# Optimization experiments

Measured on AMD Instinct MI355X. Metric: run time of the kernel, lower is better.

## Reference

```python
import jax, jax.numpy as jnp
import numpy as np

# Module config (matches init_kwargs)
IN_CH, K, N_LAYERS, STRIDE = 4, 4, 2, 2
N_QUBITS = 6           # ceil(log2(4*4*4)) = 6
DIM = 2 ** N_QUBITS    # 64 amplitudes
B, H = 128, 128


def setup_inputs() -> dict:
    key = jax.random.key(0)
    k1, k2 = jax.random.split(key)
    x = jax.random.normal(k1, (B, IN_CH, H, H), dtype=jnp.float32)
    weights = jax.random.normal(k2, (N_LAYERS, N_QUBITS, 3), dtype=jnp.float32)
    return {"x": x, "weights": weights}


def _rot(phi, theta, omega):
    # PennyLane Rot(phi, theta, omega) = RZ(omega) RY(theta) RZ(phi)
    c = jnp.cos(theta / 2).astype(jnp.complex64)
    s = jnp.sin(theta / 2).astype(jnp.complex64)
    ep = jnp.exp(-0.5j * (phi + omega).astype(jnp.complex64))
    em = jnp.exp(-0.5j * (phi - omega).astype(jnp.complex64))
    row0 = jnp.stack([ep * c, -jnp.conj(em) * s])
    row1 = jnp.stack([em * s, jnp.conj(ep) * c])
    return jnp.stack([row0, row1])  # (2,2) complex64


def _apply_1q(state, U, w):
    # state: (N, 2,...,2); wire w -> axis 1+w (wire 0 most significant)
    s = jnp.moveaxis(state, 1 + w, -1)
    s = s @ U.T
    return jnp.moveaxis(s, -1, 1 + w)


def _apply_cnot(state, c, t):
    s = jnp.moveaxis(state, (1 + c, 1 + t), (1, 2))
    s = jnp.stack([s[:, 0], s[:, 1, ::-1]], axis=1)
    return jnp.moveaxis(s, (1, 2), (1 + c, 1 + t))


def _circuit(feat, weights):
    # feat: (N, DIM) amplitude-embedded & normalized features
    state = feat.astype(jnp.complex64).reshape((-1,) + (2,) * N_QUBITS)
    ranges = [(l % (N_QUBITS - 1)) + 1 for l in range(N_LAYERS)]
    for _rep in range(N_LAYERS):  # circuit applies the full template n_layers times
        for l in range(N_LAYERS):
            for w in range(N_QUBITS):
                U = _rot(weights[l, w, 0], weights[l, w, 1], weights[l, w, 2])
                state = _apply_1q(state, U, w)
            r = ranges[l]
            for w in range(N_QUBITS):
                state = _apply_cnot(state, w, (w + r) % N_QUBITS)
    probs = state.real ** 2 + state.imag ** 2
    z = []
    for w in range(N_QUBITS):
        p = jnp.moveaxis(probs, 1 + w, 1).reshape(probs.shape[0], 2, -1)
        z.append(p[:, 0].sum(-1) - p[:, 1].sum(-1))  # <Z_w>
    return jnp.stack(z, axis=1)  # (N, n_qubits)


def reference(x, weights):
    Bx, C, Hx, Wx = x.shape
    oh = (Hx - K) // STRIDE + 1
    idx = (jnp.arange(oh) * STRIDE)[:, None] + jnp.arange(K)  # (oh, K)
    p = x[:, :, idx, :]       # (B, C, oh, K, W)
    p = p[..., idx]           # (B, C, oh, K, oh, K)
    p = jnp.transpose(p, (0, 2, 4, 1, 3, 5)).reshape(Bx * oh * oh, C * K * K)
    feat = jnp.pad(p, ((0, 0), (0, DIM - C * K * K)))  # AmplitudeEmbedding pad_with=0
    feat = feat / jnp.linalg.norm(feat, axis=1, keepdims=True)  # normalize=True
    z = _circuit(feat, weights)                        # (B*oh*oh, n_qubits)
    out = z.reshape(Bx, oh, oh, N_QUBITS).transpose(0, 3, 1, 2)
    return out  # (B, n_qubits, oh, oh)
```

## Files before the change

### kernel.cpp

```cpp
#include <hip/hip_runtime.h>

#define NQ   6
#define DIM  64
#define OH   63
#define HH   128
#define CIN  4
#define NB   128
#define PSTR 80

typedef __attribute__((ext_vector_type(8))) short short8;
typedef __attribute__((ext_vector_type(4))) float f32x4;

__device__ __forceinline__ unsigned bf16_rne_u(float f) {
    unsigned u = __builtin_bit_cast(unsigned, f);
    return (u + 0x7fffu + ((u >> 16) & 1u)) >> 16;
}

#if __has_builtin(__builtin_amdgcn_cvt_pk_bf16_f32)
__device__ __forceinline__ unsigned pk_bf16(float a, float b) {
    typedef __attribute__((ext_vector_type(2))) __bf16 bf16x2_t;
    bf16x2_t v = __builtin_amdgcn_cvt_pk_bf16_f32(a, b);
    return __builtin_bit_cast(unsigned, v);
}
#else
__device__ __forceinline__ unsigned pk_bf16(float a, float b) {
    return bf16_rne_u(a) | (bf16_rne_u(b) << 16);
}
#endif

__global__ __launch_bounds__(64) void build_u(const float* __restrict__ wts,
                                              float2* __restrict__ Ut) {
    const int i   = threadIdx.x;
    const int col = blockIdx.x;
    float2 amp = make_float2(i == col ? 1.0f : 0.0f, 0.0f);
    const int ranges[2] = {1, 2};

    for (int rep = 0; rep < 2; ++rep) {
        for (int l = 0; l < 2; ++l) {
            for (int w = 0; w < NQ; ++w) {
                const float phi = wts[(l * NQ + w) * 3 + 0];
                const float th  = wts[(l * NQ + w) * 3 + 1];
                const float om  = wts[(l * NQ + w) * 3 + 2];
                const float hc = cosf(0.5f * th);
                const float hs = sinf(0.5f * th);
                const float ap = -0.5f * (phi + om);
                const float am = -0.5f * (phi - om);
                const float2 ep = make_float2(cosf(ap), sinf(ap));
                const float2 em = make_float2(cosf(am), sinf(am));
                const float2 U00 = make_float2( ep.x * hc,  ep.y * hc);
                const float2 U01 = make_float2(-em.x * hs,  em.y * hs);
                const float2 U10 = make_float2( em.x * hs,  em.y * hs);
                const float2 U11 = make_float2( ep.x * hc, -ep.y * hc);
                const int p = 5 - w;
                const int bbit = (i >> p) & 1;
                const float px = __shfl_xor(amp.x, 1 << p, 64);
                const float py = __shfl_xor(amp.y, 1 << p, 64);
                const float2 ua = bbit ? U11 : U00;
                const float2 ub = bbit ? U10 : U01;
                float2 na;
                na.x = ua.x * amp.x - ua.y * amp.y + ub.x * px - ub.y * py;
                na.y = ua.x * amp.y + ua.y * amp.x + ub.x * py + ub.y * px;
                amp = na;
            }
            const int r = ranges[l];
            for (int w = 0; w < NQ; ++w) {
                const int pc = 5 - w;
                const int pt = 5 - ((w + r) % NQ);
                const int src = i ^ (((i >> pc) & 1) << pt);
                const float nx = __shfl(amp.x, src, 64);
                const float ny = __shfl(amp.y, src, 64);
                amp = make_float2(nx, ny);
            }
        }
    }
    Ut[col * DIM + i] = amp;
}

__global__ __launch_bounds__(64) void wprep(const float2* __restrict__ Ut,
                                            short* __restrict__ wfrag) {
    const int f = blockIdx.x;
    const int l = threadIdx.x;
    const int mt = f >> 1;
    const int t  = f & 1;
    const int m  = mt * 16 + (l & 15);
    short8 v;
#pragma unroll
    for (int j = 0; j < 8; ++j) {
        const int k = t * 32 + (l >> 4) * 8 + j;
        const float2 u = Ut[k * DIM + (m & 63)];
        const float val = (m < 64) ? u.x : u.y;
        v[j] = (short)bf16_rne_u(val);
    }
    ((int4*)wfrag)[f * 64 + l] = __builtin_bit_cast(int4, v);
}

__global__ __launch_bounds__(256, 3) void qconv_mfma(const float* __restrict__ x,
                                                     const short* __restrict__ wfrag,
                                                     float* __restrict__ out) {
    __shared__ __align__(16) short sP[4][16 * PSTR];

    const int tid  = threadIdx.x;
    const int lane = tid & 63;
    const int wv   = tid >> 6;
    const int n    = lane & 15;
    const int qq   = lane >> 4;

    const int row = blockIdx.x * 4 + wv;
    const int b   = row / OH;
    const int oy  = row - b * OH;

    const int c0  = qq >> 1;
    const int kh0 = (qq & 1) * 2;
    const float* xb  = x + (size_t)b * CIN * HH * HH;
    const float* r00 = xb + ((c0    ) * HH + 2 * oy + kh0    ) * HH;
    const float* r01 = xb + ((c0    ) * HH + 2 * oy + kh0 + 1) * HH;
    const float* r10 = xb + ((c0 + 2) * HH + 2 * oy + kh0    ) * HH;
    const float* r11 = xb + ((c0 + 2) * HH + 2 * oy + kh0 + 1) * HH;

#define LOAD8(dst, ch_)                                                      \
    {                                                                        \
        const int oxl_ = min((ch_) * 16 + n, OH - 1);                        \
        const int fo_  = 2 * oxl_;                                           \
        dst[0] = *(const float2*)(r00 + fo_);                                \
        dst[1] = *(const float2*)(r00 + fo_ + 2);                            \
        dst[2] = *(const float2*)(r01 + fo_);                                \
        dst[3] = *(const float2*)(r01 + fo_ + 2);                            \
        dst[4] = *(const float2*)(r10 + fo_);                                \
        dst[5] = *(const float2*)(r10 + fo_ + 2);                            \
        dst[6] = *(const float2*)(r11 + fo_);                                \
        dst[7] = *(const float2*)(r11 + fo_ + 2);                            \
    }

    float2 cur[8];
    LOAD8(cur, 0)

    short8 wfr[8][2];
    {
        const int4* wp = (const int4*)wfrag;
#pragma unroll
        for (int mt = 0; mt < 8; ++mt)
#pragma unroll
            for (int t = 0; t < 2; ++t)
                wfr[mt][t] = __builtin_bit_cast(short8, wp[(mt * 2 + t) * 64 + lane]);
    }

    short8 sfr[2];
#pragma unroll
    for (int t = 0; t < 2; ++t) {
        short8 v;
#pragma unroll
        for (int j = 0; j < 8; ++j) {
            const int i = t * 32 + qq * 8 + j;
            unsigned short s;
            if (n < 6)       s = ((i >> (5 - n)) & 1) ? 0xBF80 : 0x3F80;
            else if (n == 6) s = 0x3F80;
            else             s = 0;
            v[j] = (short)s;
        }
        sfr[t] = v;
    }

    short* myP = sP[wv];

#pragma unroll
    for (int ch = 0; ch < 4; ++ch) {
        float2 nxt[8];
        if (ch < 3) LOAD8(nxt, ch + 1)

        uint4 u0, u1;
        u0.x = pk_bf16(cur[0].x, cur[0].y);  u0.y = pk_bf16(cur[1].x, cur[1].y);
        u0.z = pk_bf16(cur[2].x, cur[2].y);  u0.w = pk_bf16(cur[3].x, cur[3].y);
        u1.x = pk_bf16(cur[4].x, cur[4].y);  u1.y = pk_bf16(cur[5].x, cur[5].y);
        u1.z = pk_bf16(cur[6].x, cur[6].y);  u1.w = pk_bf16(cur[7].x, cur[7].y);
        const short8 bf0 = __builtin_bit_cast(short8, u0);
        const short8 bf1 = __builtin_bit_cast(short8, u1);

        f32x4 acc[8];
#pragma unroll
        for (int mt = 0; mt < 8; ++mt) acc[mt] = (f32x4){0.f, 0.f, 0.f, 0.f};
#pragma unroll
        for (int mt = 0; mt < 8; ++mt) {
            acc[mt] = __builtin_amdgcn_mfma_f32_16x16x32_bf16(wfr[mt][0], bf0, acc[mt], 0, 0, 0);
            acc[mt] = __builtin_amdgcn_mfma_f32_16x16x32_bf16(wfr[mt][1], bf1, acc[mt], 0, 0, 0);
        }

#pragma unroll
        for (int mt = 0; mt < 4; ++mt) {
            const float p0 = acc[mt][0] * acc[mt][0] + acc[mt + 4][0] * acc[mt + 4][0];
            const float p1 = acc[mt][1] * acc[mt][1] + acc[mt + 4][1] * acc[mt + 4][1];
            const float p2 = acc[mt][2] * acc[mt][2] + acc[mt + 4][2] * acc[mt + 4][2];
            const float p3 = acc[mt][3] * acc[mt][3] + acc[mt + 4][3] * acc[mt + 4][3];
            const unsigned w0 = pk_bf16(p0, p1);
            const unsigned w1 = pk_bf16(p2, p3);
            *((uint2*)(((unsigned*)myP) + n * (PSTR / 2) + mt * 8 + qq * 2)) =
                make_uint2(w0, w1);
        }

        const short8 p0f = *(const short8*)(myP + n * PSTR + qq * 8);
        const short8 p1f = *(const short8*)(myP + n * PSTR + 32 + qq * 8);
        f32x4 c2 = (f32x4){0.f, 0.f, 0.f, 0.f};
        c2 = __builtin_amdgcn_mfma_f32_16x16x32_bf16(sfr[0], p0f, c2, 0, 0, 0);
        c2 = __builtin_amdgcn_mfma_f32_16x16x32_bf16(sfr[1], p1f, c2, 0, 0, 0);

        const float norm = __shfl(c2[2], 16 + n, 64);
        const float inv  = 1.0f / norm;
        const int ox = ch * 16 + n;
        if (ox < OH) {
            float* ob = out + ((size_t)b * NQ * OH + oy) * OH + ox;
            if (qq == 0) {
#pragma unroll
                for (int r = 0; r < 4; ++r)
                    __builtin_nontemporal_store(c2[r] * inv, ob + (size_t)r * (OH * OH));
            } else if (qq == 1) {
                __builtin_nontemporal_store(c2[0] * inv, ob + (size_t)4 * (OH * OH));
                __builtin_nontemporal_store(c2[1] * inv, ob + (size_t)5 * (OH * OH));
            }
        }

        if (ch < 3) {
#pragma unroll
            for (int i = 0; i < 8; ++i) cur[i] = nxt[i];
        }
    }
#undef LOAD8
}

extern "C" void kernel_launch(void* const* d_in, const int* in_sizes, int n_in,
                              void* d_out, int out_size, void* d_ws, size_t ws_size,
                              hipStream_t stream) {
    const float* x   = (const float*)d_in[0];
    const float* wts = (const float*)d_in[1];
    float* out = (float*)d_out;

    float2* Ut    = (float2*)d_ws;
    short*  wfrag = (short*)((char*)d_ws + 64 * 1024);

    build_u<<<64, 64, 0, stream>>>(wts, Ut);
    wprep<<<16, 64, 0, stream>>>(Ut, wfrag);
    qconv_mfma<<<(NB * OH) / 4, 256, 0, stream>>>(x, wfrag, out);
}
```

Measured before the change: 105.6 us.

## Fuse unitary build and fragment prep, split each row across two blocks

New measurement: 93.89 us (median of 2 runs). 11.1% less time.

```diff
diff --git a/kernel.cpp b/kernel.cpp
--- a/kernel.cpp
+++ b/kernel.cpp
@@ -28,41 +28,48 @@
 }
 #endif
 
-__global__ __launch_bounds__(64) void build_u(const float* __restrict__ wts,
-                                              float2* __restrict__ Ut) {
+__global__ __launch_bounds__(64) void build_wfrag(const float* __restrict__ wts,
+                                                  short* __restrict__ wfrag) {
     const int i   = threadIdx.x;
     const int col = blockIdx.x;
+
+    const int g = (i < 12) ? i : 0;
+    const float phi = wts[g * 3 + 0];
+    const float th  = wts[g * 3 + 1];
+    const float om  = wts[g * 3 + 2];
+    const float hc = cosf(0.5f * th);
+    const float hs = sinf(0.5f * th);
+    const float ap = -0.5f * (phi + om);
+    const float am = -0.5f * (phi - om);
+    const float ga = cosf(ap) * hc;
+    const float gb = sinf(ap) * hc;
+    const float gc = cosf(am) * hs;
+    const float gd = sinf(am) * hs;
+
     float2 amp = make_float2(i == col ? 1.0f : 0.0f, 0.0f);
-    const int ranges[2] = {1, 2};
 
     for (int rep = 0; rep < 2; ++rep) {
         for (int l = 0; l < 2; ++l) {
             for (int w = 0; w < NQ; ++w) {
-                const float phi = wts[(l * NQ + w) * 3 + 0];
-                const float th  = wts[(l * NQ + w) * 3 + 1];
-                const float om  = wts[(l * NQ + w) * 3 + 2];
-                const float hc = cosf(0.5f * th);
-                const float hs = sinf(0.5f * th);
-                const float ap = -0.5f * (phi + om);
-                const float am = -0.5f * (phi - om);
-                const float2 ep = make_float2(cosf(ap), sinf(ap));
-                const float2 em = make_float2(cosf(am), sinf(am));
-                const float2 U00 = make_float2( ep.x * hc,  ep.y * hc);
-                const float2 U01 = make_float2(-em.x * hs,  em.y * hs);
-                const float2 U10 = make_float2( em.x * hs,  em.y * hs);
-                const float2 U11 = make_float2( ep.x * hc, -ep.y * hc);
+                const int src = l * 6 + w;
+                const float a = __shfl(ga, src, 64);
+                const float b = __shfl(gb, src, 64);
+                const float c = __shfl(gc, src, 64);
+                const float d = __shfl(gd, src, 64);
                 const int p = 5 - w;
                 const int bbit = (i >> p) & 1;
                 const float px = __shfl_xor(amp.x, 1 << p, 64);
                 const float py = __shfl_xor(amp.y, 1 << p, 64);
-                const float2 ua = bbit ? U11 : U00;
-                const float2 ub = bbit ? U10 : U01;
+                const float uax = a;
+                const float uay = bbit ? -b : b;
+                const float ubx = bbit ? c : -c;
+                const float uby = d;
                 float2 na;
-                na.x = ua.x * amp.x - ua.y * amp.y + ub.x * px - ub.y * py;
-                na.y = ua.x * amp.y + ua.y * amp.x + ub.x * py + ub.y * px;
+                na.x = uax * amp.x - uay * amp.y + ubx * px - uby * py;
+                na.y = uax * amp.y + uay * amp.x + ubx * py + uby * px;
                 amp = na;
             }
-            const int r = ranges[l];
+            const int r = (l == 0) ? 1 : 2;
             for (int w = 0; w < NQ; ++w) {
                 const int pc = 5 - w;
                 const int pt = 5 - ((w + r) % NQ);
@@ -73,25 +80,34 @@
             }
         }
     }
-    Ut[col * DIM + i] = amp;
-}
-
-__global__ __launch_bounds__(64) void wprep(const float2* __restrict__ Ut,
-                                            short* __restrict__ wfrag) {
-    const int f = blockIdx.x;
-    const int l = threadIdx.x;
-    const int mt = f >> 1;
-    const int t  = f & 1;
-    const int m  = mt * 16 + (l & 15);
-    short8 v;
-#pragma unroll
-    for (int j = 0; j < 8; ++j) {
-        const int k = t * 32 + (l >> 4) * 8 + j;
-        const float2 u = Ut[k * DIM + (m & 63)];
-        const float val = (m < 64) ? u.x : u.y;
-        v[j] = (short)bf16_rne_u(val);
-    }
-    ((int4*)wfrag)[f * 64 + l] = __builtin_bit_cast(int4, v);
+
+    const int t    = col >> 5;
+    const int quad = (col >> 3) & 3;
+    const int j    = col & 7;
+    const int lre  = quad * 16 + (i & 15);
+    const int fre  = ((i >> 4)    ) * 2 + t;
+    const int fim  = ((i >> 4) + 4) * 2 + t;
+    wfrag[(fre * 64 + lre) * 8 + j] = (short)bf16_rne_u(amp.x);
+    wfrag[(fim * 64 + lre) * 8 + j] = (short)bf16_rne_u(amp.y);
+
+    {
+        const int n  = i & 15;
+        const int qq = i >> 4;
+#pragma unroll
+        for (int tt = 0; tt < 2; ++tt) {
+            short8 v;
+#pragma unroll
+            for (int jj = 0; jj < 8; ++jj) {
+                const int k = tt * 32 + qq * 8 + jj;
+                unsigned short s;
+                if (n < 6)       s = ((k >> (5 - n)) & 1) ? 0xBF80 : 0x3F80;
+                else if (n == 6) s = 0x3F80;
+                else             s = 0;
+                v[jj] = (short)s;
+            }
+            ((int4*)wfrag)[(16 + tt) * 64 + i] = __builtin_bit_cast(int4, v);
+        }
+    }
 }
 
 __global__ __launch_bounds__(256, 3) void qconv_mfma(const float* __restrict__ x,
@@ -105,9 +121,11 @@
     const int n    = lane & 15;
     const int qq   = lane >> 4;
 
-    const int row = blockIdx.x * 4 + wv;
-    const int b   = row / OH;
-    const int oy  = row - b * OH;
+    const int bid   = blockIdx.x;
+    const int row   = (bid >> 1) * 4 + wv;
+    const int half2 = (bid & 1) * 2;
+    const int b     = row / OH;
+    const int oy    = row - b * OH;
 
     const int c0  = qq >> 1;
     const int kh0 = (qq & 1) * 2;
@@ -117,9 +135,9 @@
     const float* r10 = xb + ((c0 + 2) * HH + 2 * oy + kh0    ) * HH;
     const float* r11 = xb + ((c0 + 2) * HH + 2 * oy + kh0 + 1) * HH;
 
-#define LOAD8(dst, ch_)                                                      \
+#define LOAD8(dst, chg_)                                                     \
     {                                                                        \
-        const int oxl_ = min((ch_) * 16 + n, OH - 1);                        \
+        const int oxl_ = min((chg_) * 16 + n, OH - 1);                       \
         const int fo_  = 2 * oxl_;                                           \
         dst[0] = *(const float2*)(r00 + fo_);                                \
         dst[1] = *(const float2*)(r00 + fo_ + 2);                            \
@@ -132,9 +150,9 @@
     }
 
     float2 cur[8];
-    LOAD8(cur, 0)
-
-    short8 wfr[8][2];
+    LOAD8(cur, half2)
+
+    short8 wfr[8][2], sfr[2];
     {
         const int4* wp = (const int4*)wfrag;
 #pragma unroll
@@ -142,30 +160,17 @@
 #pragma unroll
             for (int t = 0; t < 2; ++t)
                 wfr[mt][t] = __builtin_bit_cast(short8, wp[(mt * 2 + t) * 64 + lane]);
-    }
-
-    short8 sfr[2];
-#pragma unroll
-    for (int t = 0; t < 2; ++t) {
-        short8 v;
-#pragma unroll
-        for (int j = 0; j < 8; ++j) {
-            const int i = t * 32 + qq * 8 + j;
-            unsigned short s;
-            if (n < 6)       s = ((i >> (5 - n)) & 1) ? 0xBF80 : 0x3F80;
-            else if (n == 6) s = 0x3F80;
-            else             s = 0;
-            v[j] = (short)s;
-        }
-        sfr[t] = v;
+#pragma unroll
+        for (int t = 0; t < 2; ++t)
+            sfr[t] = __builtin_bit_cast(short8, wp[(16 + t) * 64 + lane]);
     }
 
     short* myP = sP[wv];
 
 #pragma unroll
-    for (int ch = 0; ch < 4; ++ch) {
+    for (int ch = 0; ch < 2; ++ch) {
         float2 nxt[8];
-        if (ch < 3) LOAD8(nxt, ch + 1)
+        if (ch < 1) LOAD8(nxt, half2 + 1)
 
         uint4 u0, u1;
         u0.x = pk_bf16(cur[0].x, cur[0].y);  u0.y = pk_bf16(cur[1].x, cur[1].y);
@@ -204,7 +209,7 @@
 
         const float norm = __shfl(c2[2], 16 + n, 64);
         const float inv  = 1.0f / norm;
-        const int ox = ch * 16 + n;
+        const int ox = (half2 + ch) * 16 + n;
         if (ox < OH) {
             float* ob = out + ((size_t)b * NQ * OH + oy) * OH + ox;
             if (qq == 0) {
@@ -217,7 +222,7 @@
             }
         }
 
-        if (ch < 3) {
+        if (ch < 1) {
 #pragma unroll
             for (int i = 0; i < 8; ++i) cur[i] = nxt[i];
         }
@@ -231,11 +236,8 @@
     const float* x   = (const float*)d_in[0];
     const float* wts = (const float*)d_in[1];
     float* out = (float*)d_out;
-
-    float2* Ut    = (float2*)d_ws;
-    short*  wfrag = (short*)((char*)d_ws + 64 * 1024);
-
-    build_u<<<64, 64, 0, stream>>>(wts, Ut);
-    wprep<<<16, 64, 0, stream>>>(Ut, wfrag);
-    qconv_mfma<<<(NB * OH) / 4, 256, 0, stream>>>(x, wfrag, out);
-}
+    short* wfrag = (short*)d_ws;
+
+    build_wfrag<<<64, 64, 0, stream>>>(wts, wfrag);
+    qconv_mfma<<<(NB * OH) / 2, 256, 0, stream>>>(x, wfrag, out);
+}
```
